# Performance work log

Measured on AMD Instinct MI355X. Metric: run time of the kernel, lower is better.

The kernel has to match this reference:

```python
import jax, jax.numpy as jnp
import numpy as np

N = 100000      # nodes
E = 1200000     # edges
K = 512         # TopKPooling ratio=512 -> fixed k
EPS = 1e-7      # GENConv message eps
BN_EPS = 1e-5   # BatchNorm eps
NEG_SLOPE = 0.01  # LeakyReLU default


def _lin_init(key, fan_in, fan_out):
    k1, k2 = jax.random.split(key)
    s = 1.0 / np.sqrt(fan_in)
    w = jax.random.uniform(k1, (fan_in, fan_out), minval=-s, maxval=s, dtype=jnp.float32)
    b = jax.random.uniform(k2, (fan_out,), minval=-s, maxval=s, dtype=jnp.float32)
    return w, b


def setup_inputs() -> dict:
    key = jax.random.key(0)
    ks = jax.random.split(key, 12)
    pos = jax.random.normal(ks[0], (N, 3), dtype=jnp.float32)
    edge_index = jax.random.randint(ks[1], (2, E), 0, N, dtype=jnp.int64)
    # GENConv(3, 16): lin_src + MLP [16, 32, 16] (BatchNorm+ReLU on hidden)
    c1_lw, c1_lb = _lin_init(ks[2], 3, 16)
    c1_w1, c1_b1 = _lin_init(ks[3], 16, 32)
    c1_g1 = jnp.ones((32,), jnp.float32); c1_be1 = jnp.zeros((32,), jnp.float32)
    c1_w2, c1_b2 = _lin_init(ks[4], 32, 16)
    # GENConv(16, 64): lin_src + MLP [64, 128, 64]
    c2_lw, c2_lb = _lin_init(ks[5], 16, 64)
    c2_w1, c2_b1 = _lin_init(ks[6], 64, 128)
    c2_g1 = jnp.ones((128,), jnp.float32); c2_be1 = jnp.zeros((128,), jnp.float32)
    c2_w2, c2_b2 = _lin_init(ks[7], 128, 64)
    # TopKPooling score weight [in_channels]
    pool_w = jax.random.uniform(ks[8], (64,), minval=-1.0/8, maxval=1.0/8, dtype=jnp.float32)
    return dict(pos=pos, edge_index=edge_index,
                c1_lw=c1_lw, c1_lb=c1_lb, c1_w1=c1_w1, c1_b1=c1_b1,
                c1_g1=c1_g1, c1_be1=c1_be1, c1_w2=c1_w2, c1_b2=c1_b2,
                c2_lw=c2_lw, c2_lb=c2_lb, c2_w1=c2_w1, c2_b1=c2_b1,
                c2_g1=c2_g1, c2_be1=c2_be1, c2_w2=c2_w2, c2_b2=c2_b2,
                pool_w=pool_w)


def _genconv(x, src, dst, lw, lb, w1, b1, g1, be1, w2, b2):
    # lin_src (in_channels != out_channels)
    x = x @ lw + lb                                   # [N, C]
    # message: relu(x_j) + eps
    msg = jax.nn.relu(x[src]) + EPS                   # [E, C]
    # softmax aggregation (t = 1.0), per destination, per channel
    m = jax.ops.segment_max(msg, dst, num_segments=N) # [N, C]
    a = jnp.exp(msg - m[dst])
    denom = jax.ops.segment_sum(a, dst, num_segments=N)
    alpha = a / (denom[dst] + 1e-16)
    out = jax.ops.segment_sum(msg * alpha, dst, num_segments=N)
    out = out + x                                     # residual with dst features
    # MLP: Linear -> BatchNorm (train-mode stats) -> ReLU -> Linear
    h = out @ w1 + b1
    mu = h.mean(axis=0)
    var = h.var(axis=0)
    h = (h - mu) / jnp.sqrt(var + BN_EPS) * g1 + be1
    h = jax.nn.relu(h)
    return h @ w2 + b2


def reference(pos, edge_index,
              c1_lw, c1_lb, c1_w1, c1_b1, c1_g1, c1_be1, c1_w2, c1_b2,
              c2_lw, c2_lb, c2_w1, c2_b1, c2_g1, c2_be1, c2_w2, c2_b2,
              pool_w):
    src, dst = edge_index[0], edge_index[1]
    x = _genconv(pos, src, dst, c1_lw, c1_lb, c1_w1, c1_b1, c1_g1, c1_be1, c1_w2, c1_b2)
    x = jnp.where(x > 0, x, NEG_SLOPE * x)            # LeakyReLU
    x = _genconv(x, src, dst, c2_lw, c2_lb, c2_w1, c2_b1, c2_g1, c2_be1, c2_w2, c2_b2)
    x = jnp.where(x > 0, x, NEG_SLOPE * x)
    # TopKPooling: score = tanh(x . w / ||w||), select top K, gate selected features
    score = jnp.tanh((x @ pool_w) / jnp.linalg.norm(pool_w))  # [N]
    top_vals, perm = jax.lax.top_k(score, K)
    return x[perm] * top_vals[:, None]                # [K, 64]
```

## Files before the change

kernel.cpp:

```cpp
#include <hip/hip_runtime.h>
#include <stdint.h>

#define BLK 256

static constexpr float F_EPS = 1e-7f;
static constexpr float F_NEG = 0.01f;
static constexpr int   TOPK  = 512;
static constexpr int   PA    = 128;
static constexpr int   BSH   = 9;
static constexpr int   MAXBUK= 256;
static constexpr int   CAP   = 8192;

typedef unsigned long long u64;

__device__ __forceinline__ unsigned int ord_f32(float f) {
  unsigned int u = __float_as_uint(f);
  return (u & 0x80000000u) ? ~u : (u | 0x80000000u);
}

template<int CIN, int COUT, int TM, bool BN, bool LEAKY, bool STAT>
__global__ __launch_bounds__(256) void gemm_tile(const float* __restrict__ in,
    const float* __restrict__ W, const float* __restrict__ b,
    const float* __restrict__ scale, const float* __restrict__ shift,
    float* __restrict__ out, double* __restrict__ partial, int n) {
  constexpr int TN = COUT / 16;
  constexpr int NODES = 16 * TM;
  constexpr int KC = (CIN > 64) ? 64 : CIN;
  constexpr int NPAD = NODES + 4;
  __shared__ float xs[KC][NPAD];
  __shared__ float wsh[CIN * COUT];
  __shared__ float sB[COUT];
  __shared__ float sSc[BN ? CIN : 4];
  __shared__ float sSh[BN ? CIN : 4];
  for (int i = threadIdx.x; i < CIN * COUT; i += 256) wsh[i] = W[i];
  for (int i = threadIdx.x; i < COUT; i += 256) sB[i] = b[i];
  if constexpr (BN) {
    for (int i = threadIdx.x; i < CIN; i += 256) { sSc[i] = scale[i]; sSh[i] = shift[i]; }
  }
  __syncthreads();
  const int tn = threadIdx.x & 15;
  const int tj = threadIdx.x >> 4;
  const int node0 = blockIdx.x * NODES;

  float acc[TM][TN];
  #pragma unroll
  for (int m = 0; m < TM; ++m)
    #pragma unroll
    for (int j = 0; j < TN; ++j) acc[m][j] = sB[tj * TN + j];

  for (int kc = 0; kc < CIN; kc += KC) {
    __syncthreads();
    constexpr int NL = NODES * (KC / 4);
    for (int i = threadIdx.x; i < NL; i += 256) {
      int nd = i / (KC / 4);
      int kq = i - nd * (KC / 4);
      int gn = node0 + nd;
      const float* p = in + (size_t)(gn < n ? gn : n - 1) * CIN + kc + kq * 4;
      float4 v = *reinterpret_cast<const float4*>(p);
      if constexpr (BN) {
        int kb = kc + kq * 4;
        v.x = fmaxf(v.x * sSc[kb+0] + sSh[kb+0], 0.f);
        v.y = fmaxf(v.y * sSc[kb+1] + sSh[kb+1], 0.f);
        v.z = fmaxf(v.z * sSc[kb+2] + sSh[kb+2], 0.f);
        v.w = fmaxf(v.w * sSc[kb+3] + sSh[kb+3], 0.f);
      }
      xs[kq*4+0][nd] = v.x; xs[kq*4+1][nd] = v.y;
      xs[kq*4+2][nd] = v.z; xs[kq*4+3][nd] = v.w;
    }
    __syncthreads();
    #pragma unroll 16
    for (int k = 0; k < KC; ++k) {
      float xv[TM], wv[TN];
      #pragma unroll
      for (int m = 0; m < TM; ++m) xv[m] = xs[k][tn * TM + m];
      #pragma unroll
      for (int j = 0; j < TN; ++j) wv[j] = wsh[(kc + k) * COUT + tj * TN + j];
      #pragma unroll
      for (int m = 0; m < TM; ++m)
        #pragma unroll
        for (int j = 0; j < TN; ++j)
          acc[m][j] += xv[m] * wv[j];
    }
  }
  #pragma unroll
  for (int m = 0; m < TM; ++m) {
    int gn = node0 + tn * TM + m;
    if (gn < n) {
      float* orow = out + (size_t)gn * COUT + tj * TN;
      #pragma unroll
      for (int j = 0; j < TN; j += 4) {
        float a0 = acc[m][j], a1 = acc[m][j+1], a2 = acc[m][j+2], a3 = acc[m][j+3];
        if constexpr (LEAKY) {
          a0 = a0 > 0.f ? a0 : F_NEG * a0;
          a1 = a1 > 0.f ? a1 : F_NEG * a1;
          a2 = a2 > 0.f ? a2 : F_NEG * a2;
          a3 = a3 > 0.f ? a3 : F_NEG * a3;
        }
        float4 r; r.x = a0; r.y = a1; r.z = a2; r.w = a3;
        *reinterpret_cast<float4*>(orow + j) = r;
      }
    }
  }
  if constexpr (STAT) {
    __shared__ double sStat[2 * COUT];
    double sv[TN], qv[TN];
    #pragma unroll
    for (int j = 0; j < TN; ++j) { sv[j] = 0.0; qv[j] = 0.0; }
    #pragma unroll
    for (int m = 0; m < TM; ++m) {
      bool v = (node0 + tn * TM + m) < n;
      #pragma unroll
      for (int j = 0; j < TN; ++j) {
        double a = v ? (double)acc[m][j] : 0.0;
        sv[j] += a; qv[j] += a * a;
      }
    }
    #pragma unroll
    for (int j = 0; j < TN; ++j) {
      for (int off = 8; off; off >>= 1) {
        sv[j] += __shfl_down(sv[j], off, 16);
        qv[j] += __shfl_down(qv[j], off, 16);
      }
    }
    if (tn == 0) {
      #pragma unroll
      for (int j = 0; j < TN; ++j) {
        sStat[tj * TN + j] = sv[j];
        sStat[COUT + tj * TN + j] = qv[j];
      }
    }
    __syncthreads();
    for (int i = threadIdx.x; i < 2 * COUT; i += 256)
      partial[(size_t)blockIdx.x * (2 * COUT) + i] = sStat[i];
  }
}

template<int COUT>
__global__ __launch_bounds__(256) void bn_fin_ws(const double* __restrict__ partial,
    const float* __restrict__ g, const float* __restrict__ be,
    float* __restrict__ sc, float* __restrict__ sh, int n, int nbx) {
  int j = blockIdx.x;
  int t = threadIdx.x;
  double s = 0, q = 0;
  for (int bdx = t; bdx < nbx; bdx += 256) {
    s += partial[(size_t)bdx * (2 * COUT) + j];
    q += partial[(size_t)bdx * (2 * COUT) + COUT + j];
  }
  for (int off = 32; off; off >>= 1) { s += __shfl_down(s, off); q += __shfl_down(q, off); }
  __shared__ double sw[4][2];
  int lane = t & 63, wid = t >> 6;
  if (lane == 0) { sw[wid][0] = s; sw[wid][1] = q; }
  __syncthreads();
  if (t == 0) {
    s = sw[0][0] + sw[1][0] + sw[2][0] + sw[3][0];
    q = sw[0][1] + sw[1][1] + sw[2][1] + sw[3][1];
    double inv_n = 1.0 / (double)n;
    double mu = s * inv_n;
    double var = q * inv_n - mu * mu;
    double scd = (double)g[j] / sqrt(var + 1e-5);
    sc[j] = (float)scd;
    sh[j] = (float)((double)be[j] - mu * scd);
  }
}

template<int CIN, int COUT, int JT, bool STAT = false>
__global__ __launch_bounds__(BLK) void lin_kernel(const float* __restrict__ in,
    const float* __restrict__ W, const float* __restrict__ b,
    float* __restrict__ out, double* __restrict__ partial, int n) {
  __shared__ float sW[CIN * JT];
  __shared__ float sB[JT];
  const int j0 = blockIdx.y * JT;
  for (int i = threadIdx.x; i < CIN * JT; i += BLK) {
    int k = i / JT, jj = i - k * JT;
    sW[i] = W[k * COUT + j0 + jj];
  }
  for (int i = threadIdx.x; i < JT; i += BLK) sB[i] = b[j0 + i];
  __syncthreads();
  int node = blockIdx.x * BLK + threadIdx.x;
  bool valid = node < n;
  if constexpr (!STAT) { if (!valid) return; }
  int rnode = valid ? node : (n - 1);
  float acc[JT];
  #pragma unroll
  for (int jj = 0; jj < JT; ++jj) acc[jj] = sB[jj];
  const float* xrow = in + (size_t)rnode * CIN;
  if constexpr ((CIN & 3) == 0) {
    float x[CIN];
    #pragma unroll
    for (int k4 = 0; k4 < CIN / 4; ++k4) {
      float4 v = *reinterpret_cast<const float4*>(xrow + k4 * 4);
      x[4*k4+0] = v.x; x[4*k4+1] = v.y; x[4*k4+2] = v.z; x[4*k4+3] = v.w;
    }
    #pragma unroll
    for (int k = 0; k < CIN; ++k) {
      #pragma unroll
      for (int jj = 0; jj < JT; ++jj)
        acc[jj] += x[k] * sW[k * JT + jj];
    }
  } else {
    #pragma unroll
    for (int k = 0; k < CIN; ++k) {
      float xv = xrow[k];
      #pragma unroll
      for (int jj = 0; jj < JT; ++jj)
        acc[jj] += xv * sW[k * JT + jj];
    }
  }
  if (valid) {
    float* orow = out + (size_t)node * COUT + j0;
    #pragma unroll
    for (int jj = 0; jj < JT; jj += 4) {
      float4 r; r.x = acc[jj]; r.y = acc[jj+1]; r.z = acc[jj+2]; r.w = acc[jj+3];
      *reinterpret_cast<float4*>(orow + jj) = r;
    }
  }
  if constexpr (STAT) {
    __shared__ double sStat[4][2 * JT];
    int lane = threadIdx.x & 63, wid = threadIdx.x >> 6;
    #pragma unroll
    for (int jj = 0; jj < JT; ++jj) {
      double sv = valid ? (double)acc[jj] : 0.0;
      double qv = sv * sv;
      for (int off = 32; off; off >>= 1) {
        sv += __shfl_down(sv, off);
        qv += __shfl_down(qv, off);
      }
      if (lane == 0) { sStat[wid][jj] = sv; sStat[wid][JT + jj] = qv; }
    }
    __syncthreads();
    if (threadIdx.x < 2 * JT) {
      double v = sStat[0][threadIdx.x] + sStat[1][threadIdx.x]
               + sStat[2][threadIdx.x] + sStat[3][threadIdx.x];
      partial[((size_t)blockIdx.y * gridDim.x + blockIdx.x) * (2 * JT) + threadIdx.x] = v;
    }
  }
}

template<int COUT, int JT>
__global__ __launch_bounds__(256) void bn_fin3(const double* __restrict__ partial,
    const float* __restrict__ g, const float* __restrict__ be,
    float* __restrict__ sc, float* __restrict__ sh, int n, int nbx) {
  int j = blockIdx.x;
  int t = threadIdx.x;
  int jt = j / JT, jj = j - jt * JT;
  double s = 0, q = 0;
  for (int b = t; b < nbx; b += 256) {
    const double* row = partial + ((size_t)jt * nbx + b) * (2 * JT);
    s += row[jj];
    q += row[JT + jj];
  }
  for (int off = 32; off; off >>= 1) { s += __shfl_down(s, off); q += __shfl_down(q, off); }
  __shared__ double sw[4][2];
  int lane = t & 63, wid = t >> 6;
  if (lane == 0) { sw[wid][0] = s; sw[wid][1] = q; }
  __syncthreads();
  if (t == 0) {
    s = sw[0][0] + sw[1][0] + sw[2][0] + sw[3][0];
    q = sw[0][1] + sw[1][1] + sw[2][1] + sw[3][1];
    double inv_n = 1.0 / (double)n;
    double mu = s * inv_n;
    double var = q * inv_n - mu * mu;
    double scd = (double)g[j] / sqrt(var + 1e-5);
    sc[j] = (float)scd;
    sh[j] = (float)((double)be[j] - mu * scd);
  }
}

template<int CIN, int COUT, int JT>
__global__ __launch_bounds__(BLK) void mlp2_kernel(const float* __restrict__ h,
    const float* __restrict__ scale, const float* __restrict__ shift,
    const float* __restrict__ W, const float* __restrict__ b,
    float* __restrict__ out, int n) {
  __shared__ float sW[CIN * JT];
  __shared__ float sB[JT];
  __shared__ float sSc[CIN];
  __shared__ float sSh[CIN];
  const int j0 = blockIdx.y * JT;
  for (int i = threadIdx.x; i < CIN * JT; i += BLK) {
    int k = i / JT, jj = i - k * JT;
    sW[i] = W[k * COUT + j0 + jj];
  }
  for (int i = threadIdx.x; i < JT; i += BLK) sB[i] = b[j0 + i];
  for (int i = threadIdx.x; i < CIN; i += BLK) { sSc[i] = scale[i]; sSh[i] = shift[i]; }
  __syncthreads();
  int node = blockIdx.x * BLK + threadIdx.x;
  if (node >= n) return;
  float acc[JT];
  #pragma unroll
  for (int jj = 0; jj < JT; ++jj) acc[jj] = sB[jj];
  const float* xrow = h + (size_t)node * CIN;
  float x[CIN];
  #pragma unroll
  for (int k4 = 0; k4 < CIN / 4; ++k4) {
    float4 v = *reinterpret_cast<const float4*>(xrow + k4 * 4);
    x[4*k4+0] = fmaxf(v.x * sSc[4*k4+0] + sSh[4*k4+0], 0.f);
    x[4*k4+1] = fmaxf(v.y * sSc[4*k4+1] + sSh[4*k4+1], 0.f);
    x[4*k4+2] = fmaxf(v.z * sSc[4*k4+2] + sSh[4*k4+2], 0.f);
    x[4*k4+3] = fmaxf(v.w * sSc[4*k4+3] + sSh[4*k4+3], 0.f);
  }
  #pragma unroll
  for (int k = 0; k < CIN; ++k) {
    #pragma unroll
    for (int jj = 0; jj < JT; ++jj)
      acc[jj] += x[k] * sW[k * JT + jj];
  }
  float* orow = out + (size_t)node * COUT + j0;
  #pragma unroll
  for (int jj = 0; jj < JT; jj += 4) {
    float a0 = acc[jj], a1 = acc[jj+1], a2 = acc[jj+2], a3 = acc[jj+3];
    a0 = a0 > 0.f ? a0 : F_NEG * a0;
    a1 = a1 > 0.f ? a1 : F_NEG * a1;
    a2 = a2 > 0.f ? a2 : F_NEG * a2;
    a3 = a3 > 0.f ? a3 : F_NEG * a3;
    float4 r; r.x = a0; r.y = a1; r.z = a2; r.w = a3;
    *reinterpret_cast<float4*>(orow + jj) = r;
  }
}

__global__ __launch_bounds__(BLK) void deg_kernel(const int* __restrict__ dst,
    int* __restrict__ deg, int E) {
  int e = blockIdx.x * BLK + threadIdx.x;
  if (e < E) atomicAdd(&deg[dst[e]], 1);
}

__global__ __launch_bounds__(BLK) void blocksum_kernel(const int* __restrict__ deg,
    int* __restrict__ bsum, int n) {
  int i = blockIdx.x * BLK + threadIdx.x;
  int v = (i < n) ? deg[i] : 0;
  for (int off = 32; off; off >>= 1) v += __shfl_down(v, off);
  __shared__ int wsum[4];
  int lane = threadIdx.x & 63, wid = threadIdx.x >> 6;
  if (lane == 0) wsum[wid] = v;
  __syncthreads();
  if (threadIdx.x == 0) bsum[blockIdx.x] = wsum[0] + wsum[1] + wsum[2] + wsum[3];
}

__global__ __launch_bounds__(512) void scanb_kernel(int* __restrict__ bsum, int nb) {
  __shared__ int s[512];
  int t = threadIdx.x;
  int orig = (t < nb) ? bsum[t] : 0;
  s[t] = orig;
  __syncthreads();
  for (int off = 1; off < 512; off <<= 1) {
    int add = (t >= off) ? s[t - off] : 0;
    __syncthreads();
    s[t] += add;
    __syncthreads();
  }
  if (t < nb) bsum[t] = s[t] - orig;
}

__global__ __launch_bounds__(BLK) void rowstart_kernel(const int* __restrict__ deg,
    const int* __restrict__ bsum, int* __restrict__ rowstart, int n) {
  __shared__ int s[BLK];
  int t = threadIdx.x, i = blockIdx.x * BLK + t;
  int orig = (i < n) ? deg[i] : 0;
  s[t] = orig;
  __syncthreads();
  for (int off = 1; off < BLK; off <<= 1) {
    int add = (t >= off) ? s[t - off] : 0;
    __syncthreads();
    s[t] += add;
    __syncthreads();
  }
  if (i < n) rowstart[i] = bsum[blockIdx.x] + s[t] - orig;
}

__global__ __launch_bounds__(BLK) void pcount_kernel(const int* __restrict__ dst,
    int* __restrict__ pcnt, int E, int chunk) {
  __shared__ int cb[MAXBUK];
  for (int i = threadIdx.x; i < MAXBUK; i += BLK) cb[i] = 0;
  __syncthreads();
  int e0 = blockIdx.x * chunk;
  int e1 = min(e0 + chunk, E);
  for (int e = e0 + threadIdx.x; e < e1; e += BLK)
    atomicAdd(&cb[dst[e] >> BSH], 1);
  __syncthreads();
  for (int i = threadIdx.x; i < MAXBUK; i += BLK)
    pcnt[blockIdx.x * MAXBUK + i] = cb[i];
}

__global__ __launch_bounds__(256) void pscan_kernel(const int* __restrict__ pcnt,
    int* __restrict__ poff, int* __restrict__ ptot, int nblk, int nbuk) {
  __shared__ int s[256];
  __shared__ int tot[256];
  int t = threadIdx.x;
  int sum = 0;
  if (t < nbuk) {
    for (int blk = 0; blk < nblk; ++blk) {
      int v = pcnt[blk * MAXBUK + t];
      poff[blk * MAXBUK + t] = sum;
      sum += v;
    }
  }
  tot[t] = (t < nbuk) ? sum : 0;
  s[t] = tot[t];
  __syncthreads();
  for (int off = 1; off < 256; off <<= 1) {
    int add = (t >= off) ? s[t - off] : 0;
    __syncthreads();
    s[t] += add;
    __syncthreads();
  }
  if (t < nbuk) ptot[t] = s[t] - tot[t];
  if (t == 0) ptot[nbuk] = s[255];
}

__global__ __launch_bounds__(BLK) void ppack_kernel(const int* __restrict__ src,
    const int* __restrict__ dst, const int* __restrict__ poff,
    const int* __restrict__ ptot, int* __restrict__ pairbuf, int E, int chunk) {
  __shared__ int cb[MAXBUK];
  for (int i = threadIdx.x; i < MAXBUK; i += BLK)
    cb[i] = ptot[i] + poff[blockIdx.x * MAXBUK + i];
  __syncthreads();
  int e0 = blockIdx.x * chunk;
  int e1 = min(e0 + chunk, E);
  for (int e = e0 + threadIdx.x; e < e1; e += BLK) {
    int d = dst[e], sv = src[e];
    int b = d >> BSH;
    int pos = atomicAdd(&cb[b], 1);
    pairbuf[pos] = ((d & ((1 << BSH) - 1)) << 17) | sv;
  }
}

__global__ __launch_bounds__(BLK) void place_kernel(const int* __restrict__ pairbuf,
    const int* __restrict__ ptot, const int* __restrict__ rowstart,
    int* __restrict__ eidx, int n, int E) {
  __shared__ int lcur[1 << BSH];
  __shared__ int seg[CAP];
  const int b = blockIdx.x;
  const int n0 = b << BSH;
  const int nn = min(1 << BSH, n - n0);
  const int base = rowstart[n0];
  const int segend = (n0 + (1 << BSH) >= n) ? E : rowstart[n0 + (1 << BSH)];
  const int seglen = segend - base;
  for (int i = threadIdx.x; i < nn; i += BLK)
    lcur[i] = rowstart[n0 + i] - base;
  __syncthreads();
  const int p0 = ptot[b], p1 = ptot[b + 1];
  if (seglen <= CAP) {
    for (int i = p0 + threadIdx.x; i < p1; i += BLK) {
      int pk = pairbuf[i];
      int dloc = pk >> 17;
      int pos = atomicAdd(&lcur[dloc], 1);
      seg[pos] = pk & 0x1FFFF;
    }
    __syncthreads();
    for (int i = threadIdx.x; i < seglen; i += BLK)
      eidx[base + i] = seg[i];
  } else {
    for (int i = p0 + threadIdx.x; i < p1; i += BLK) {
      int pk = pairbuf[i];
      int dloc = pk >> 17;
      int pos = atomicAdd(&lcur[dloc], 1);
      eidx[base + pos] = pk & 0x1FFFF;
    }
  }
}

template<int C>
__global__ __launch_bounds__(BLK) void agg_kernel(const int* __restrict__ rowstart,
    const int* __restrict__ deg, const int* __restrict__ eidx,
    const float* __restrict__ x, float* __restrict__ out, int n) {
  int gid = blockIdx.x * BLK + threadIdx.x;
  int node, c;
  if constexpr (C == 64) {
    node = __builtin_amdgcn_readfirstlane(gid >> 6);
    c = threadIdx.x & 63;
  } else {
    node = gid / C;
    c = gid & (C - 1);
  }
  if (node >= n) return;
  int s0, d;
  if constexpr (C == 64) {
    s0 = __builtin_amdgcn_readfirstlane(rowstart[node]);
    d  = __builtin_amdgcn_readfirstlane(deg[node]);
  } else {
    s0 = rowstart[node];
    d  = deg[node];
  }
  const float* xc = x + c;
  const int* ep = eidx + s0;
  float den = 0.f, num = 0.f;
  int nq = d >> 2;
  int i0 = 0, i1 = 0, i2 = 0, i3 = 0;
  int j0 = 0, j1 = 0, j2 = 0, j3 = 0;
  if (nq > 0) { i0 = ep[0]; i1 = ep[1]; i2 = ep[2]; i3 = ep[3]; }
  if (nq > 1) { j0 = ep[4]; j1 = ep[5]; j2 = ep[6]; j3 = ep[7]; }
  int q = 0;
  for (; q + 1 < nq; q += 2) {
    float xa = xc[(unsigned)i0 * C];
    float xb = xc[(unsigned)i1 * C];
    float xcv = xc[(unsigned)i2 * C];
    float xd = xc[(unsigned)i3 * C];
    float ya = xc[(unsigned)j0 * C];
    float yb = xc[(unsigned)j1 * C];
    float yc = xc[(unsigned)j2 * C];
    float yd = xc[(unsigned)j3 * C];
    if (q + 2 < nq) {
      const int* p2 = ep + (q + 2) * 4;
      i0 = p2[0]; i1 = p2[1]; i2 = p2[2]; i3 = p2[3];
    }
    if (q + 3 < nq) {
      const int* p3 = ep + (q + 3) * 4;
      j0 = p3[0]; j1 = p3[1]; j2 = p3[2]; j3 = p3[3];
    }
    float ma = fmaxf(xa, 0.f) + F_EPS;
    float mb = fmaxf(xb, 0.f) + F_EPS;
    float mc = fmaxf(xcv, 0.f) + F_EPS;
    float md = fmaxf(xd, 0.f) + F_EPS;
    float na = fmaxf(ya, 0.f) + F_EPS;
    float nb = fmaxf(yb, 0.f) + F_EPS;
    float nc = fmaxf(yc, 0.f) + F_EPS;
    float nd = fmaxf(yd, 0.f) + F_EPS;
    float aa = __expf(ma), ab = __expf(mb), ac = __expf(mc), ad = __expf(md);
    float ba = __expf(na), bb = __expf(nb), bc = __expf(nc), bd = __expf(nd);
    den += ((aa + ab) + (ac + ad)) + ((ba + bb) + (bc + bd));
    num += ((ma * aa + mb * ab) + (mc * ac + md * ad))
         + ((na * ba + nb * bb) + (nc * bc + nd * bd));
  }
  if (q < nq) {
    float xa = xc[(unsigned)i0 * C];
    float xb = xc[(unsigned)i1 * C];
    float xcv = xc[(unsigned)i2 * C];
    float xd = xc[(unsigned)i3 * C];
    float ma = fmaxf(xa, 0.f) + F_EPS;
    float mb = fmaxf(xb, 0.f) + F_EPS;
    float mc = fmaxf(xcv, 0.f) + F_EPS;
    float md = fmaxf(xd, 0.f) + F_EPS;
    float aa = __expf(ma), ab = __expf(mb), ac = __expf(mc), ad = __expf(md);
    den += (aa + ab) + (ac + ad);
    num += (ma * aa + mb * ab) + (mc * ac + md * ad);
  }
  for (int j = nq * 4; j < d; ++j) {
    int sA = ep[j];
    float xa = xc[(unsigned)sA * C];
    float ma = fmaxf(xa, 0.f) + F_EPS;
    float aa = __expf(ma);
    den += aa;
    num += ma * aa;
  }
  float xdv = xc[(unsigned)node * C];
  out[(size_t)node * C + c] = num / (den + 1e-16f) + xdv;
}

__global__ __launch_bounds__(BLK) void score_kernel(const float* __restrict__ x,
    const float* __restrict__ w, float* __restrict__ scores,
    u64* __restrict__ keys, int* __restrict__ ghist, int n) {
  __shared__ float sw[64];
  __shared__ float snorm;
  __shared__ int hl[256];
  if (threadIdx.x < 64) sw[threadIdx.x] = w[threadIdx.x];
  hl[threadIdx.x] = 0;
  __syncthreads();
  if (threadIdx.x < 64) {
    float v = sw[threadIdx.x];
    float sq = v * v;
    for (int off = 32; off; off >>= 1) sq += __shfl_down(sq, off);
    if (threadIdx.x == 0) snorm = 1.f / sqrtf(sq);
  }
  __syncthreads();
  int node = blockIdx.x * BLK + threadIdx.x;
  if (node < n) {
    const float4* row = reinterpret_cast<const float4*>(x + (size_t)node * 64);
    float acc = 0.f;
    #pragma unroll
    for (int k4 = 0; k4 < 16; ++k4) {
      float4 v = row[k4];
      const float4 wv = *reinterpret_cast<const float4*>(&sw[4 * k4]);
      acc += v.x * wv.x + v.y * wv.y + v.z * wv.z + v.w * wv.w;
    }
    float s = tanhf(acc * snorm);
    scores[node] = s;
    u64 key = ((u64)ord_f32(s) << 17) | (u64)(0x1FFFF - node);
    keys[node] = key;
    atomicAdd(&hl[(int)(key >> 41)], 1);
  }
  __syncthreads();
  int v = hl[threadIdx.x];
  if (v) atomicAdd(&ghist[threadIdx.x], v);
}

__global__ void pick0_kernel(int* __restrict__ istate, const int* __restrict__ hist) {
  if (threadIdx.x == 0) {
    int k = TOPK, run = 0;
    for (int d = 255; d >= 0; --d) {
      int c = hist[d];
      if (run + c >= k) { istate[1] = d; istate[0] = k - run; break; }
      run += c;
    }
    istate[2] = 0; istate[4] = 0;
  }
}

__global__ __launch_bounds__(BLK) void compact0_kernel(const u64* __restrict__ in,
    u64* __restrict__ outb, u64* __restrict__ sel, int* __restrict__ istate, int n) {
  int i = blockIdx.x * BLK + threadIdx.x;
  if (i >= n) return;
  u64 kkey = in[i];
  int b = (int)(kkey >> 41);
  int digit = istate[1];
  if (b > digit) {
    sel[atomicAdd(&istate[2], 1)] = kkey;
  } else if (b == digit) {
    outb[atomicAdd(&istate[4], 1)] = kkey;
  }
}

__global__ __launch_bounds__(1024) void topk_finish(u64* __restrict__ bufB,
    u64* __restrict__ bufA, u64* __restrict__ sel, const int* __restrict__ istate,
    const float* __restrict__ scores, int* __restrict__ perm,
    float* __restrict__ gval) {
  __shared__ int hl[512];
  __shared__ int tsum[512];
  __shared__ u64 sk[512];
  __shared__ int sh_digit, sh_k, sh_sel, sh_out, sh_cnt;
  int t = threadIdx.x;
  if (t == 0) { sh_cnt = istate[4]; sh_k = istate[0]; sh_sel = istate[2]; }
  __syncthreads();
  u64* cur = bufB;
  u64* nxt = bufA;
  const int shifts[5] = {33, 25, 17, 9, 0};
  const int masks[5]  = {255, 255, 255, 255, 511};
  for (int r = 0; r < 5; ++r) {
    const int shift = shifts[r], mask = masks[r], wlen = mask + 1;
    for (int i = t; i < wlen; i += 1024) hl[i] = 0;
    __syncthreads();
    int cnt = sh_cnt, krem = sh_k;
    for (int i = t; i < cnt; i += 1024)
      atomicAdd(&hl[(int)(cur[i] >> shift) & mask], 1);
    __syncthreads();
    int v = 0;
    if (t < wlen) { v = hl[t]; tsum[t] = v; }
    __syncthreads();
    for (int off = 1; off < wlen; off <<= 1) {
      int add = 0;
      if (t + off < wlen) add = tsum[t + off];
      __syncthreads();
      if (t + off < wlen) tsum[t] += add;
      __syncthreads();
    }
    if (t < wlen) {
      int T = tsum[t];
      if (T >= krem && (T - v) < krem) {
        sh_digit = t;
        sh_k = krem - (T - v);
      }
    }
    if (t == 0) sh_out = 0;
    __syncthreads();
    int digit = sh_digit;
    for (int i = t; i < cnt; i += 1024) {
      u64 kk = cur[i];
      int b = (int)(kk >> shift) & mask;
      if (b > digit) sel[atomicAdd(&sh_sel, 1)] = kk;
      else if (b == digit) nxt[atomicAdd(&sh_out, 1)] = kk;
    }
    __syncthreads();
    if (t == 0) sh_cnt = sh_out;
    __syncthreads();
    u64* tmp = cur; cur = nxt; nxt = tmp;
  }
  int base = sh_sel, krem = sh_k;
  for (int i = t; i < krem; i += 1024) sel[base + i] = cur[i];
  __syncthreads();
  if (t < 512) sk[t] = sel[t];
  __syncthreads();
  if (t < 512) {
    u64 key = sk[t];
    int rank = 0;
    for (int j = 0; j < 512; ++j) rank += (sk[j] > key) ? 1 : 0;
    int node = 0x1FFFF - (int)(key & 0x1FFFFull);
    perm[rank] = node;
    gval[rank] = scores[node];
  }
}

__global__ __launch_bounds__(256) void gather_kernel(const int* __restrict__ perm,
    const float* __restrict__ gval, const float* __restrict__ x,
    float* __restrict__ out) {
  int i = blockIdx.x * 256 + threadIdx.x;
  int r = i >> 4, c = i & 15;
  int node = perm[r];
  float v = gval[r];
  float4 xv = reinterpret_cast<const float4*>(x)[(size_t)node * 16 + c];
  float4 o; o.x = xv.x * v; o.y = xv.y * v; o.z = xv.z * v; o.w = xv.w * v;
  reinterpret_cast<float4*>(out)[(size_t)r * 16 + c] = o;
}

extern "C" void kernel_launch(void* const* d_in, const int* in_sizes, int n_in,
                              void* d_out, int out_size, void* d_ws, size_t ws_size,
                              hipStream_t stream) {
  const int N = in_sizes[0] / 3;
  const int E = in_sizes[1] / 2;

  const float* pos   = (const float*)d_in[0];
  const int*   ei    = (const int*)d_in[1];
  const int*   src   = ei;
  const int*   dst   = ei + E;
  const float* c1_lw = (const float*)d_in[2];
  const float* c1_lb = (const float*)d_in[3];
  const float* c1_w1 = (const float*)d_in[4];
  const float* c1_b1 = (const float*)d_in[5];
  const float* c1_g1 = (const float*)d_in[6];
  const float* c1_be1= (const float*)d_in[7];
  const float* c1_w2 = (const float*)d_in[8];
  const float* c1_b2 = (const float*)d_in[9];
  const float* c2_lw = (const float*)d_in[10];
  const float* c2_lb = (const float*)d_in[11];
  const float* c2_w1 = (const float*)d_in[12];
  const float* c2_b1 = (const float*)d_in[13];
  const float* c2_g1 = (const float*)d_in[14];
  const float* c2_be1= (const float*)d_in[15];
  const float* c2_w2 = (const float*)d_in[16];
  const float* c2_b2 = (const float*)d_in[17];
  const float* poolw = (const float*)d_in[18];

  float* ws = (float*)d_ws;
  float* x1   = ws;
  float* h1   = ws + (size_t)16 * N;
  float* o1   = ws + (size_t)48 * N;
  float* res2 = ws;
  float* x2   = ws + (size_t)64 * N;
  float* res1 = x2;
  float* h2   = ws + (size_t)128 * N;
  float* o2   = ws + (size_t)256 * N;
  float* scores = ws + (size_t)320 * N;
  u64* candA = (u64*)(ws + (size_t)321 * N);
  u64* candB = candA + N;
  u64* sel   = candB + N;
  double* partial = (double*)(sel + TOPK);
  int* ibase   = (int*)(partial + (size_t)524288);
  int* istate  = ibase;
  int* hist    = ibase + 8;
  int* bsum    = ibase + 264;
  int* perm    = ibase + 776;
  float* gval  = (float*)(ibase + 1288);
  int* deg     = ibase + 1800;
  int* rowstart= deg + N;
  int* eidx    = rowstart + N;
  int* pairbuf = eidx + E;
  int* pcnt    = pairbuf + E;
  int* poff    = pcnt + PA * MAXBUK;
  int* ptot    = poff + PA * MAXBUK;
  float* fsc   = (float*)(ptot + MAXBUK + 1);
  float* sc1 = fsc;        float* sh1 = fsc + 32;
  float* sc2 = fsc + 64;   float* sh2 = fsc + 192;

  const int nbN = (N + BLK - 1) / BLK;
  const int nbE = (E + BLK - 1) / BLK;
  const int nbG = (N + 63) / 64;
  const int NBUK = (N + (1 << BSH) - 1) >> BSH;
  const int chunk = (E + PA - 1) / PA;

  hipMemsetAsync(ibase, 0, (size_t)(1800 + N) * sizeof(int), stream);

  deg_kernel<<<nbE, BLK, 0, stream>>>(dst, deg, E);
  blocksum_kernel<<<nbN, BLK, 0, stream>>>(deg, bsum, N);
  scanb_kernel<<<1, 512, 0, stream>>>(bsum, nbN);
  rowstart_kernel<<<nbN, BLK, 0, stream>>>(deg, bsum, rowstart, N);
  pcount_kernel<<<PA, BLK, 0, stream>>>(dst, pcnt, E, chunk);
  pscan_kernel<<<1, 256, 0, stream>>>(pcnt, poff, ptot, PA, NBUK);
  ppack_kernel<<<PA, BLK, 0, stream>>>(src, dst, poff, ptot, pairbuf, E, chunk);
  place_kernel<<<NBUK, BLK, 0, stream>>>(pairbuf, ptot, rowstart, eidx, N, E);

  lin_kernel<3, 16, 16><<<dim3(nbN, 1), BLK, 0, stream>>>(pos, c1_lw, c1_lb, x1, nullptr, N);
  agg_kernel<16><<<(N * 16 + BLK - 1) / BLK, BLK, 0, stream>>>(rowstart, deg, eidx, x1, res1, N);
  lin_kernel<16, 32, 32, true><<<dim3(nbN, 1), BLK, 0, stream>>>(res1, c1_w1, c1_b1, h1, partial, N);
  bn_fin3<32, 32><<<32, 256, 0, stream>>>(partial, c1_g1, c1_be1, sc1, sh1, N, nbN);
  mlp2_kernel<32, 16, 16><<<dim3(nbN, 1), BLK, 0, stream>>>(h1, sc1, sh1, c1_w2, c1_b2, o1, N);

  gemm_tile<16, 64, 4, false, false, false><<<nbG, 256, 0, stream>>>(
      o1, c2_lw, c2_lb, nullptr, nullptr, x2, nullptr, N);
  agg_kernel<64><<<(N * 64 + BLK - 1) / BLK, BLK, 0, stream>>>(rowstart, deg, eidx, x2, res2, N);
  gemm_tile<64, 128, 4, false, false, true><<<nbG, 256, 0, stream>>>(
      res2, c2_w1, c2_b1, nullptr, nullptr, h2, partial, N);
  bn_fin_ws<128><<<128, 256, 0, stream>>>(partial, c2_g1, c2_be1, sc2, sh2, N, nbG);
  gemm_tile<128, 64, 4, true, true, false><<<nbG, 256, 0, stream>>>(
      h2, c2_w2, c2_b2, sc2, sh2, o2, nullptr, N);

  score_kernel<<<nbN, BLK, 0, stream>>>(o2, poolw, scores, candA, hist, N);
  pick0_kernel<<<1, 64, 0, stream>>>(istate, hist);
  compact0_kernel<<<nbN, BLK, 0, stream>>>(candA, candB, sel, istate, N);
  topk_finish<<<1, 1024, 0, stream>>>(candB, candA, sel, istate, scores, perm, gval);
  gather_kernel<<<32, 256, 0, stream>>>(perm, gval, o2, (float*)d_out);

  (void)n_in; (void)out_size; (void)ws_size;
}
```

Measured before the change: 395.5 us.

## Derive degree and row starts inside bucket place kernel, drop separate CSR passes

Removes the global-atomic degree kernel and the three-kernel prefix scan that built row starts. The place kernel now counts destinations per bucket in shared memory, scans them locally, and writes deg and rowstart itself, using the bucket offsets already computed. This cuts four launches, a large memset, and 1.2M global atomics, in exchange for an extra pass over pairbuf and a shared-memory scan per bucket.

After: 342.3 us. 1.16x faster.

```diff
diff --git a/kernel.cpp b/kernel.cpp
--- a/kernel.cpp
+++ b/kernel.cpp
@@ -317,55 +317,6 @@
   }
 }
 
-__global__ __launch_bounds__(BLK) void deg_kernel(const int* __restrict__ dst,
-    int* __restrict__ deg, int E) {
-  int e = blockIdx.x * BLK + threadIdx.x;
-  if (e < E) atomicAdd(&deg[dst[e]], 1);
-}
-
-__global__ __launch_bounds__(BLK) void blocksum_kernel(const int* __restrict__ deg,
-    int* __restrict__ bsum, int n) {
-  int i = blockIdx.x * BLK + threadIdx.x;
-  int v = (i < n) ? deg[i] : 0;
-  for (int off = 32; off; off >>= 1) v += __shfl_down(v, off);
-  __shared__ int wsum[4];
-  int lane = threadIdx.x & 63, wid = threadIdx.x >> 6;
-  if (lane == 0) wsum[wid] = v;
-  __syncthreads();
-  if (threadIdx.x == 0) bsum[blockIdx.x] = wsum[0] + wsum[1] + wsum[2] + wsum[3];
-}
-
-__global__ __launch_bounds__(512) void scanb_kernel(int* __restrict__ bsum, int nb) {
-  __shared__ int s[512];
-  int t = threadIdx.x;
-  int orig = (t < nb) ? bsum[t] : 0;
-  s[t] = orig;
-  __syncthreads();
-  for (int off = 1; off < 512; off <<= 1) {
-    int add = (t >= off) ? s[t - off] : 0;
-    __syncthreads();
-    s[t] += add;
-    __syncthreads();
-  }
-  if (t < nb) bsum[t] = s[t] - orig;
-}
-
-__global__ __launch_bounds__(BLK) void rowstart_kernel(const int* __restrict__ deg,
-    const int* __restrict__ bsum, int* __restrict__ rowstart, int n) {
-  __shared__ int s[BLK];
-  int t = threadIdx.x, i = blockIdx.x * BLK + t;
-  int orig = (i < n) ? deg[i] : 0;
-  s[t] = orig;
-  __syncthreads();
-  for (int off = 1; off < BLK; off <<= 1) {
-    int add = (t >= off) ? s[t - off] : 0;
-    __syncthreads();
-    s[t] += add;
-    __syncthreads();
-  }
-  if (i < n) rowstart[i] = bsum[blockIdx.x] + s[t] - orig;
-}
-
 __global__ __launch_bounds__(BLK) void pcount_kernel(const int* __restrict__ dst,
     int* __restrict__ pcnt, int E, int chunk) {
   __shared__ int cb[MAXBUK];
@@ -424,36 +375,59 @@
 }
 
 __global__ __launch_bounds__(BLK) void place_kernel(const int* __restrict__ pairbuf,
-    const int* __restrict__ ptot, const int* __restrict__ rowstart,
-    int* __restrict__ eidx, int n, int E) {
+    const int* __restrict__ ptot, int* __restrict__ deg, int* __restrict__ rowstart,
+    int* __restrict__ eidx, int n) {
+  __shared__ int cnt[1 << BSH];
+  __shared__ int scn[1 << BSH];
   __shared__ int lcur[1 << BSH];
   __shared__ int seg[CAP];
   const int b = blockIdx.x;
   const int n0 = b << BSH;
   const int nn = min(1 << BSH, n - n0);
-  const int base = rowstart[n0];
-  const int segend = (n0 + (1 << BSH) >= n) ? E : rowstart[n0 + (1 << BSH)];
-  const int seglen = segend - base;
-  for (int i = threadIdx.x; i < nn; i += BLK)
-    lcur[i] = rowstart[n0 + i] - base;
-  __syncthreads();
   const int p0 = ptot[b], p1 = ptot[b + 1];
+  const int seglen = p1 - p0;
+  for (int i = threadIdx.x; i < (1 << BSH); i += BLK) cnt[i] = 0;
+  __syncthreads();
+  for (int i = p0 + threadIdx.x; i < p1; i += BLK)
+    atomicAdd(&cnt[pairbuf[i] >> 17], 1);
+  __syncthreads();
+  {
+    int i0 = threadIdx.x, i1 = threadIdx.x + 256;
+    scn[i0] = cnt[i0];
+    scn[i1] = cnt[i1];
+    __syncthreads();
+    for (int off = 1; off < (1 << BSH); off <<= 1) {
+      int v0 = (i0 >= off) ? scn[i0 - off] : 0;
+      int v1 = (i1 >= off) ? scn[i1 - off] : 0;
+      __syncthreads();
+      scn[i0] += v0;
+      scn[i1] += v1;
+      __syncthreads();
+    }
+  }
+  for (int i = threadIdx.x; i < (1 << BSH); i += BLK) {
+    int excl = scn[i] - cnt[i];
+    lcur[i] = excl;
+    if (i < nn) {
+      deg[n0 + i] = cnt[i];
+      rowstart[n0 + i] = p0 + excl;
+    }
+  }
+  __syncthreads();
   if (seglen <= CAP) {
     for (int i = p0 + threadIdx.x; i < p1; i += BLK) {
       int pk = pairbuf[i];
-      int dloc = pk >> 17;
-      int pos = atomicAdd(&lcur[dloc], 1);
+      int pos = atomicAdd(&lcur[pk >> 17], 1);
       seg[pos] = pk & 0x1FFFF;
     }
     __syncthreads();
     for (int i = threadIdx.x; i < seglen; i += BLK)
-      eidx[base + i] = seg[i];
+      eidx[p0 + i] = seg[i];
   } else {
     for (int i = p0 + threadIdx.x; i < p1; i += BLK) {
       int pk = pairbuf[i];
-      int dloc = pk >> 17;
-      int pos = atomicAdd(&lcur[dloc], 1);
-      eidx[base + pos] = pk & 0x1FFFF;
+      int pos = atomicAdd(&lcur[pk >> 17], 1);
+      eidx[p0 + pos] = pk & 0x1FFFF;
     }
   }
 }
@@ -734,7 +708,6 @@
   int* ibase   = (int*)(partial + (size_t)524288);
   int* istate  = ibase;
   int* hist    = ibase + 8;
-  int* bsum    = ibase + 264;
   int* perm    = ibase + 776;
   float* gval  = (float*)(ibase + 1288);
   int* deg     = ibase + 1800;
@@ -749,21 +722,16 @@
   float* sc2 = fsc + 64;   float* sh2 = fsc + 192;
 
   const int nbN = (N + BLK - 1) / BLK;
-  const int nbE = (E + BLK - 1) / BLK;
   const int nbG = (N + 63) / 64;
   const int NBUK = (N + (1 << BSH) - 1) >> BSH;
   const int chunk = (E + PA - 1) / PA;
 
-  hipMemsetAsync(ibase, 0, (size_t)(1800 + N) * sizeof(int), stream);
-
-  deg_kernel<<<nbE, BLK, 0, stream>>>(dst, deg, E);
-  blocksum_kernel<<<nbN, BLK, 0, stream>>>(deg, bsum, N);
-  scanb_kernel<<<1, 512, 0, stream>>>(bsum, nbN);
-  rowstart_kernel<<<nbN, BLK, 0, stream>>>(deg, bsum, rowstart, N);
+  hipMemsetAsync(ibase, 0, 1800 * sizeof(int), stream);
+
   pcount_kernel<<<PA, BLK, 0, stream>>>(dst, pcnt, E, chunk);
   pscan_kernel<<<1, 256, 0, stream>>>(pcnt, poff, ptot, PA, NBUK);
   ppack_kernel<<<PA, BLK, 0, stream>>>(src, dst, poff, ptot, pairbuf, E, chunk);
-  place_kernel<<<NBUK, BLK, 0, stream>>>(pairbuf, ptot, rowstart, eidx, N, E);
+  place_kernel<<<NBUK, BLK, 0, stream>>>(pairbuf, ptot, deg, rowstart, eidx, N);
 
   lin_kernel<3, 16, 16><<<dim3(nbN, 1), BLK, 0, stream>>>(pos, c1_lw, c1_lb, x1, nullptr, N);
   agg_kernel<16><<<(N * 16 + BLK - 1) / BLK, BLK, 0, stream>>>(rowstart, deg, eidx, x1, res1, N);
```
